# Kernel optimization log

Measured on AMD Instinct MI355X. Metric: run time of the kernel, lower is better.

The kernel has to match this reference:

```python
import jax, jax.numpy as jnp
import numpy as np

B, H, S, D = 4, 16, 2048, 128


def setup_inputs() -> dict:
    key = jax.random.key(0)
    kq, kk, kv, km = jax.random.split(key, 4)
    queries = jax.random.normal(kq, (B, H, S, D), dtype=jnp.float32)
    keys = jax.random.normal(kk, (B, H, S, D), dtype=jnp.float32)
    values = jax.random.normal(kv, (B, H, S, D), dtype=jnp.float32)
    # 0/1 float mask (1 = masked position), broadcast over heads
    mask = jax.random.randint(km, (B, 1, S, S), 0, 2).astype(jnp.float32)
    return {"queries": queries, "keys": keys, "values": values, "mask": mask}


def reference(queries, keys, values, mask):
    dk = jnp.asarray(keys.shape[-1], dtype=queries.dtype)
    # NOTE: original code divides by dk, not sqrt(dk) — kept faithful.
    scores = jnp.einsum("bhqd,bhkd->bhqk", queries, keys) / dk
    scores = scores + mask * jnp.asarray(-1e9, dtype=scores.dtype)
    attn = jax.nn.softmax(scores, axis=-1)
    out = jnp.einsum("bhqk,bhkd->bhqd", attn, values)
    return out, attn
```

## Files before the change

kernel.cpp:

```cpp
#include <hip/hip_runtime.h>

#define Bb 4
#define Hh 16
#define Ss 2048
#define Dd 128

typedef __bf16 bf16x8 __attribute__((ext_vector_type(8)));
typedef __bf16 bf16x4 __attribute__((ext_vector_type(4)));
typedef float f32x4 __attribute__((ext_vector_type(4)));

__global__ void k_cvt(const float4* __restrict__ Q, const float4* __restrict__ K,
                      bf16x4* __restrict__ Qb, bf16x4* __restrict__ Kb) {
    size_t i = (size_t)blockIdx.x * 256 + threadIdx.x;
    float4 q = Q[i], k = K[i];
    Qb[i] = (bf16x4){(__bf16)q.x, (__bf16)q.y, (__bf16)q.z, (__bf16)q.w};
    Kb[i] = (bf16x4){(__bf16)k.x, (__bf16)k.y, (__bf16)k.z, (__bf16)k.w};
}

__global__ void k_vt(const float* __restrict__ V, __bf16* __restrict__ VT) {
    __shared__ __bf16 lds[64][65];
    int k0 = blockIdx.x * 64, d0 = blockIdx.y * 64, bh = blockIdx.z;
    int t = threadIdx.x;
    for (int i = 0; i < 16; ++i) {
        int idx = i * 256 + t;
        int kl = idx >> 6, dl = idx & 63;
        lds[kl][dl] = (__bf16)V[((size_t)(bh * Ss + k0 + kl)) * Dd + d0 + dl];
    }
    __syncthreads();
    for (int i = 0; i < 16; ++i) {
        int idx = i * 256 + t;
        int dl = idx >> 6, kl = idx & 63;
        VT[((size_t)(bh * Dd + d0 + dl)) * Ss + k0 + kl] = lds[kl][dl];
    }
}

__global__ void k_mask(const float* __restrict__ M, unsigned* __restrict__ maskT) {
    __shared__ unsigned char lds[64][68];
    int k0 = blockIdx.x * 64, q0 = blockIdx.y * 64, b = blockIdx.z;
    int t = threadIdx.x;
    for (int i = 0; i < 16; ++i) {
        int idx = i * 256 + t;
        int ql = idx >> 6, kl = idx & 63;
        lds[ql][kl] = (M[((size_t)(b * Ss + q0 + ql)) * Ss + k0 + kl] != 0.0f) ? 1 : 0;
    }
    __syncthreads();
    if (t < 128) {
        int kl = t >> 1, wsel = t & 1;
        unsigned wv = 0;
        for (int j = 0; j < 32; ++j)
            wv |= ((unsigned)lds[wsel * 32 + j][kl]) << j;
        maskT[((size_t)(b * Ss + k0 + kl)) * (Ss / 32) + (q0 >> 5) + wsel] = wv;
    }
}

__global__ __launch_bounds__(256, 2) void attn_kernel(
    const __bf16* __restrict__ Qb, const __bf16* __restrict__ Kb,
    const __bf16* __restrict__ VTb, const unsigned* __restrict__ maskT,
    float* __restrict__ out, float* __restrict__ attn) {
    __shared__ __align__(16) __bf16 Qs[64][136];
    __shared__ __align__(16) __bf16 Ks[64][136];
    __shared__ __align__(16) __bf16 VTs[128][72];
    __shared__ __align__(16) __bf16 Ps[4][16][72];
    __shared__ float linv[64];

    const int t = threadIdx.x;
    const int w = t >> 6, lane = t & 63, quad = lane >> 4, l16 = lane & 15;
    const int bh = blockIdx.y, b = bh >> 4;
    const int q0 = blockIdx.x << 6;

    {
        const int row = t >> 4, col = (t & 15) << 3;
        for (int p = 0; p < 4; ++p) {
            int r = p * 16 + row;
            float4 v = *(const float4*)(Qb + ((size_t)(bh * Ss + q0 + r)) * Dd + col);
            *(float4*)&Qs[r][col] = v;
        }
    }
    const int qw = (q0 >> 5) + (w >> 1);
    const int bitbase = ((w & 1) << 4) + (quad << 2);

    __syncthreads();
    bf16x8 aq[4];
    for (int kd = 0; kd < 4; ++kd)
        aq[kd] = *(const bf16x8*)&Qs[w * 16 + l16][kd * 32 + quad * 8];

    float rsum[4] = {0.f, 0.f, 0.f, 0.f};

    for (int k0 = 0; k0 < Ss; k0 += 64) {
        __syncthreads();
        {
            const int row = t >> 4, col = (t & 15) << 3;
            for (int p = 0; p < 4; ++p) {
                int r = p * 16 + row;
                float4 v = *(const float4*)(Kb + ((size_t)(bh * Ss + k0 + r)) * Dd + col);
                *(float4*)&Ks[r][col] = v;
            }
        }
        __syncthreads();
        for (int nt = 0; nt < 4; ++nt) {
            f32x4 acc = {0.f, 0.f, 0.f, 0.f};
            for (int kd = 0; kd < 4; ++kd) {
                bf16x8 bk = *(const bf16x8*)&Ks[nt * 16 + l16][kd * 32 + quad * 8];
                acc = __builtin_amdgcn_mfma_f32_16x16x32_bf16(aq[kd], bk, acc, 0, 0, 0);
            }
            int col = k0 + nt * 16 + l16;
            unsigned mw = maskT[((size_t)(b * Ss + col)) * (Ss / 32) + qw];
            for (int r = 0; r < 4; ++r) {
                float p = ((mw >> (bitbase + r)) & 1u) ? 0.0f
                                                       : __expf(acc[r] * 0.0078125f);
                rsum[r] += p;
            }
        }
    }
    for (int r = 0; r < 4; ++r) {
        float v = rsum[r];
        v += __shfl_xor(v, 1, 16);
        v += __shfl_xor(v, 2, 16);
        v += __shfl_xor(v, 4, 16);
        v += __shfl_xor(v, 8, 16);
        rsum[r] = v;
    }
    if (l16 == 0)
        for (int r = 0; r < 4; ++r)
            linv[w * 16 + quad * 4 + r] = 1.0f / rsum[r];
    __syncthreads();
    float li[4];
    for (int r = 0; r < 4; ++r) li[r] = linv[w * 16 + quad * 4 + r];

    f32x4 oacc[8];
    for (int d = 0; d < 8; ++d) oacc[d] = (f32x4){0.f, 0.f, 0.f, 0.f};

    for (int k0 = 0; k0 < Ss; k0 += 64) {
        __syncthreads();
        {
            const int row = t >> 4, col = (t & 15) << 3;
            for (int p = 0; p < 4; ++p) {
                int r = p * 16 + row;
                float4 v = *(const float4*)(Kb + ((size_t)(bh * Ss + k0 + r)) * Dd + col);
                *(float4*)&Ks[r][col] = v;
            }
            const int vrow = t >> 3, vcol = (t & 7) << 3;
            for (int p = 0; p < 4; ++p) {
                int r = p * 32 + vrow;
                float4 v = *(const float4*)(VTb + ((size_t)(bh * Dd + r)) * Ss + k0 + vcol);
                *(float4*)&VTs[r][vcol] = v;
            }
        }
        __syncthreads();
        for (int nt = 0; nt < 4; ++nt) {
            f32x4 acc = {0.f, 0.f, 0.f, 0.f};
            for (int kd = 0; kd < 4; ++kd) {
                bf16x8 bk = *(const bf16x8*)&Ks[nt * 16 + l16][kd * 32 + quad * 8];
                acc = __builtin_amdgcn_mfma_f32_16x16x32_bf16(aq[kd], bk, acc, 0, 0, 0);
            }
            int col = k0 + nt * 16 + l16;
            unsigned mw = maskT[((size_t)(b * Ss + col)) * (Ss / 32) + qw];
            for (int r = 0; r < 4; ++r) {
                float p = ((mw >> (bitbase + r)) & 1u)
                              ? 0.0f
                              : __expf(acc[r] * 0.0078125f) * li[r];
                attn[((size_t)(bh * Ss + q0 + w * 16 + quad * 4 + r)) * Ss + col] = p;
                Ps[w][quad * 4 + r][nt * 16 + l16] = (__bf16)p;
            }
        }
        for (int kg = 0; kg < 2; ++kg) {
            bf16x8 ap = *(const bf16x8*)&Ps[w][l16][kg * 32 + quad * 8];
            for (int dg = 0; dg < 8; ++dg) {
                bf16x8 bv = *(const bf16x8*)&VTs[dg * 16 + l16][kg * 32 + quad * 8];
                oacc[dg] = __builtin_amdgcn_mfma_f32_16x16x32_bf16(ap, bv, oacc[dg], 0, 0, 0);
            }
        }
    }
    for (int dg = 0; dg < 8; ++dg)
        for (int r = 0; r < 4; ++r)
            out[((size_t)(bh * Ss + q0 + w * 16 + quad * 4 + r)) * Dd + dg * 16 + l16] =
                oacc[dg][r];
}

extern "C" void kernel_launch(void* const* d_in, const int* in_sizes, int n_in,
                              void* d_out, int out_size, void* d_ws, size_t ws_size,
                              hipStream_t stream) {
    const float* Q = (const float*)d_in[0];
    const float* K = (const float*)d_in[1];
    const float* V = (const float*)d_in[2];
    const float* M = (const float*)d_in[3];

    float* out = (float*)d_out;
    float* attn = out + (size_t)Bb * Hh * Ss * Dd;

    char* ws = (char*)d_ws;
    __bf16* Qb = (__bf16*)ws;
    __bf16* Kb = (__bf16*)(ws + 33554432);
    __bf16* VTb = (__bf16*)(ws + 67108864);
    unsigned* maskT = (unsigned*)(ws + 100663296);

    k_cvt<<<16384, 256, 0, stream>>>((const float4*)Q, (const float4*)K,
                                     (bf16x4*)Qb, (bf16x4*)Kb);
    k_vt<<<dim3(32, 2, 64), 256, 0, stream>>>(V, VTb);
    k_mask<<<dim3(32, 32, 4), 256, 0, stream>>>(M, maskT);
    attn_kernel<<<dim3(32, 64), 256, 0, stream>>>(Qb, Kb, VTb, maskT, out, attn);
}
```

Before: 1.813 ms.

## Double-buffer K/V tiles with direct global-to-LDS loads and swizzled layout

Rewrites the attention kernel's staging so K and V^T tiles of 32 keys are double-buffered in LDS and loaded with global_load_lds, letting the next tile's load run alongside the current tile's MFMAs. LDS rows are XOR-swizzled in place of padding, Q is loaded straight into registers, and the per-row reciprocal is computed in registers without an LDS round trip. Smaller LDS use allows 4 blocks per CU, and the workgroup index is remapped so neighbouring blocks share a head. The risks are more barriers per key, since the tiles are half as large, and higher register pressure under the tighter launch bound.

Measured after the change: 1.784 ms. No clear change (-1.6%).

```diff
diff --git a/kernel.cpp b/kernel.cpp
--- a/kernel.cpp
+++ b/kernel.cpp
@@ -4,6 +4,8 @@
 #define Hh 16
 #define Ss 2048
 #define Dd 128
+#define KT 32
+#define NIT (Ss / KT)
 
 typedef __bf16 bf16x8 __attribute__((ext_vector_type(8)));
 typedef __bf16 bf16x4 __attribute__((ext_vector_type(4)));
@@ -53,128 +55,169 @@
     }
 }
 
-__global__ __launch_bounds__(256, 2) void attn_kernel(
+__device__ __forceinline__ void gl2lds16(const void* g, void* l) {
+    __builtin_amdgcn_global_load_lds(
+        (const __attribute__((address_space(1))) unsigned int*)g,
+        (__attribute__((address_space(3))) unsigned int*)l, 16, 0, 0);
+}
+
+__global__ __launch_bounds__(256, 4) void attn_kernel(
     const __bf16* __restrict__ Qb, const __bf16* __restrict__ Kb,
     const __bf16* __restrict__ VTb, const unsigned* __restrict__ maskT,
     float* __restrict__ out, float* __restrict__ attn) {
-    __shared__ __align__(16) __bf16 Qs[64][136];
-    __shared__ __align__(16) __bf16 Ks[64][136];
-    __shared__ __align__(16) __bf16 VTs[128][72];
-    __shared__ __align__(16) __bf16 Ps[4][16][72];
-    __shared__ float linv[64];
+    __shared__ __align__(16) __bf16 Ks[2][KT][Dd];
+    __shared__ __align__(16) __bf16 VTs[2][Dd][KT];
+    __shared__ __align__(16) __bf16 Ps[4][16][64];
 
     const int t = threadIdx.x;
     const int w = t >> 6, lane = t & 63, quad = lane >> 4, l16 = lane & 15;
-    const int bh = blockIdx.y, b = bh >> 4;
-    const int q0 = blockIdx.x << 6;
-
+
+    const int wg = (int)blockIdx.x + ((int)blockIdx.y << 5);
+    const int nid = ((wg & 7) << 8) + (wg >> 3);
+    const int q0 = (nid & 31) << 6;
+    const int bh = nid >> 5;
+    const int b = bh >> 4;
+
+    const __bf16* Kbh = Kb + (size_t)bh * (Ss * Dd);
+    const char* Vbh = (const char*)(VTb + (size_t)bh * ((size_t)Dd * Ss));
+
+    const int ksub = t >> 4;
+    const int kcb = ((t & 15) << 4) ^ ((ksub & 7) << 4);
+    const int vsub = t >> 2;
+    const int vcb = ((t & 3) << 4) ^ ((vsub & 3) << 4);
+    char* ldsKbase = (char*)&Ks[0][0][0] + (w << 10);
+    char* ldsVbase = (char*)&VTs[0][0][0] + (w << 10);
+
+#define STAGE_K(buf, k0_)                                                      \
+    {                                                                          \
+        const char* gb = (const char*)(Kbh + (size_t)(k0_) * Dd) + kcb;        \
+        _Pragma("unroll") for (int i_ = 0; i_ < 2; ++i_)                       \
+            gl2lds16(gb + ((i_ << 4) + ksub) * 256,                            \
+                     ldsKbase + ((buf) << 13) + (i_ << 12));                   \
+    }
+#define STAGE_V(buf, k0_)                                                      \
+    {                                                                          \
+        const char* gb = Vbh + (size_t)(k0_) * 2 + vcb;                        \
+        _Pragma("unroll") for (int i_ = 0; i_ < 2; ++i_)                       \
+            gl2lds16(gb + (size_t)((i_ << 6) + vsub) * (Ss * 2),               \
+                     ldsVbase + ((buf) << 13) + (i_ << 12));                   \
+    }
+
+    bf16x8 aq[4];
     {
-        const int row = t >> 4, col = (t & 15) << 3;
-        for (int p = 0; p < 4; ++p) {
-            int r = p * 16 + row;
-            float4 v = *(const float4*)(Qb + ((size_t)(bh * Ss + q0 + r)) * Dd + col);
-            *(float4*)&Qs[r][col] = v;
-        }
-    }
+        STAGE_K(0, 0);
+        const __bf16* qp =
+            Qb + ((size_t)(bh * Ss + q0 + (w << 4) + l16)) * Dd + (quad << 3);
+#pragma unroll
+        for (int kd = 0; kd < 4; ++kd) aq[kd] = *(const bf16x8*)(qp + (kd << 5));
+    }
+    __syncthreads();
+
+    const char* ldsK0 = (const char*)&Ks[0][0][0];
+    const char* ldsV0 = (const char*)&VTs[0][0][0];
+    const int kswz = (l16 & 7) << 4;
+    const int vswz = (l16 & 3) << 4;
+
     const int qw = (q0 >> 5) + (w >> 1);
     const int bitbase = ((w & 1) << 4) + (quad << 2);
-
-    __syncthreads();
-    bf16x8 aq[4];
-    for (int kd = 0; kd < 4; ++kd)
-        aq[kd] = *(const bf16x8*)&Qs[w * 16 + l16][kd * 32 + quad * 8];
+    const size_t mrowbase = (size_t)b * Ss * (Ss / 32);
 
     float rsum[4] = {0.f, 0.f, 0.f, 0.f};
-
-    for (int k0 = 0; k0 < Ss; k0 += 64) {
+    for (int it = 0; it < NIT; ++it) {
+        const int cur = it & 1;
+        if (it < NIT - 1) {
+            STAGE_K(cur ^ 1, (it + 1) * KT);
+        } else {
+            STAGE_K(cur ^ 1, 0);
+            STAGE_V(cur ^ 1, 0);
+        }
+        const int k0 = it * KT;
+#pragma unroll
+        for (int nt = 0; nt < 2; ++nt) {
+            f32x4 acc = {0.f, 0.f, 0.f, 0.f};
+#pragma unroll
+            for (int kd = 0; kd < 4; ++kd) {
+                bf16x8 bk = *(const bf16x8*)(ldsK0 + (cur << 13) +
+                                             ((nt * 16 + l16) << 8) +
+                                             (((kd << 6) + (quad << 4)) ^ kswz));
+                acc = __builtin_amdgcn_mfma_f32_16x16x32_bf16(aq[kd], bk, acc, 0, 0, 0);
+            }
+            const int col = k0 + nt * 16 + l16;
+            const unsigned mw = maskT[mrowbase + (size_t)col * (Ss / 32) + qw];
+#pragma unroll
+            for (int r = 0; r < 4; ++r)
+                rsum[r] += ((mw >> (bitbase + r)) & 1u) ? 0.f
+                                                        : __expf(acc[r] * 0.0078125f);
+        }
         __syncthreads();
-        {
-            const int row = t >> 4, col = (t & 15) << 3;
-            for (int p = 0; p < 4; ++p) {
-                int r = p * 16 + row;
-                float4 v = *(const float4*)(Kb + ((size_t)(bh * Ss + k0 + r)) * Dd + col);
-                *(float4*)&Ks[r][col] = v;
-            }
-        }
-        __syncthreads();
-        for (int nt = 0; nt < 4; ++nt) {
-            f32x4 acc = {0.f, 0.f, 0.f, 0.f};
-            for (int kd = 0; kd < 4; ++kd) {
-                bf16x8 bk = *(const bf16x8*)&Ks[nt * 16 + l16][kd * 32 + quad * 8];
-                acc = __builtin_amdgcn_mfma_f32_16x16x32_bf16(aq[kd], bk, acc, 0, 0, 0);
-            }
-            int col = k0 + nt * 16 + l16;
-            unsigned mw = maskT[((size_t)(b * Ss + col)) * (Ss / 32) + qw];
-            for (int r = 0; r < 4; ++r) {
-                float p = ((mw >> (bitbase + r)) & 1u) ? 0.0f
-                                                       : __expf(acc[r] * 0.0078125f);
-                rsum[r] += p;
-            }
-        }
-    }
+    }
+
+    float li[4];
+#pragma unroll
     for (int r = 0; r < 4; ++r) {
         float v = rsum[r];
         v += __shfl_xor(v, 1, 16);
         v += __shfl_xor(v, 2, 16);
         v += __shfl_xor(v, 4, 16);
         v += __shfl_xor(v, 8, 16);
-        rsum[r] = v;
-    }
-    if (l16 == 0)
-        for (int r = 0; r < 4; ++r)
-            linv[w * 16 + quad * 4 + r] = 1.0f / rsum[r];
-    __syncthreads();
-    float li[4];
-    for (int r = 0; r < 4; ++r) li[r] = linv[w * 16 + quad * 4 + r];
+        li[r] = 1.0f / v;
+    }
 
     f32x4 oacc[8];
-    for (int d = 0; d < 8; ++d) oacc[d] = (f32x4){0.f, 0.f, 0.f, 0.f};
-
-    for (int k0 = 0; k0 < Ss; k0 += 64) {
-        __syncthreads();
-        {
-            const int row = t >> 4, col = (t & 15) << 3;
-            for (int p = 0; p < 4; ++p) {
-                int r = p * 16 + row;
-                float4 v = *(const float4*)(Kb + ((size_t)(bh * Ss + k0 + r)) * Dd + col);
-                *(float4*)&Ks[r][col] = v;
-            }
-            const int vrow = t >> 3, vcol = (t & 7) << 3;
-            for (int p = 0; p < 4; ++p) {
-                int r = p * 32 + vrow;
-                float4 v = *(const float4*)(VTb + ((size_t)(bh * Dd + r)) * Ss + k0 + vcol);
-                *(float4*)&VTs[r][vcol] = v;
-            }
-        }
-        __syncthreads();
-        for (int nt = 0; nt < 4; ++nt) {
+#pragma unroll
+    for (int dg = 0; dg < 8; ++dg) oacc[dg] = (f32x4){0.f, 0.f, 0.f, 0.f};
+
+    char* myPs = (char*)&Ps[0][0][0] + (w << 11);
+
+    for (int it = 0; it < NIT; ++it) {
+        const int cur = it & 1;
+        if (it < NIT - 1) {
+            STAGE_K(cur ^ 1, (it + 1) * KT);
+            STAGE_V(cur ^ 1, (it + 1) * KT);
+        }
+        const int k0 = it * KT;
+#pragma unroll
+        for (int nt = 0; nt < 2; ++nt) {
             f32x4 acc = {0.f, 0.f, 0.f, 0.f};
+#pragma unroll
             for (int kd = 0; kd < 4; ++kd) {
-                bf16x8 bk = *(const bf16x8*)&Ks[nt * 16 + l16][kd * 32 + quad * 8];
+                bf16x8 bk = *(const bf16x8*)(ldsK0 + (cur << 13) +
+                                             ((nt * 16 + l16) << 8) +
+                                             (((kd << 6) + (quad << 4)) ^ kswz));
                 acc = __builtin_amdgcn_mfma_f32_16x16x32_bf16(aq[kd], bk, acc, 0, 0, 0);
             }
-            int col = k0 + nt * 16 + l16;
-            unsigned mw = maskT[((size_t)(b * Ss + col)) * (Ss / 32) + qw];
+            const int col = k0 + nt * 16 + l16;
+            const unsigned mw = maskT[mrowbase + (size_t)col * (Ss / 32) + qw];
+#pragma unroll
             for (int r = 0; r < 4; ++r) {
+                const int prow = (quad << 2) + r;
                 float p = ((mw >> (bitbase + r)) & 1u)
                               ? 0.0f
                               : __expf(acc[r] * 0.0078125f) * li[r];
-                attn[((size_t)(bh * Ss + q0 + w * 16 + quad * 4 + r)) * Ss + col] = p;
-                Ps[w][quad * 4 + r][nt * 16 + l16] = (__bf16)p;
-            }
-        }
-        for (int kg = 0; kg < 2; ++kg) {
-            bf16x8 ap = *(const bf16x8*)&Ps[w][l16][kg * 32 + quad * 8];
+                attn[((size_t)(bh * Ss + q0 + (w << 4) + prow)) * Ss + col] = p;
+                *(__bf16*)(myPs + (prow << 7) +
+                           ((nt * 32 + (l16 << 1)) ^ ((prow & 7) << 4))) = (__bf16)p;
+            }
+        }
+        {
+            bf16x8 ap = *(const bf16x8*)(myPs + (l16 << 7) + ((quad << 4) ^ kswz));
+#pragma unroll
             for (int dg = 0; dg < 8; ++dg) {
-                bf16x8 bv = *(const bf16x8*)&VTs[dg * 16 + l16][kg * 32 + quad * 8];
+                bf16x8 bv = *(const bf16x8*)(ldsV0 + (cur << 13) +
+                                             ((dg * 16 + l16) << 6) +
+                                             ((quad << 4) ^ vswz));
                 oacc[dg] = __builtin_amdgcn_mfma_f32_16x16x32_bf16(ap, bv, oacc[dg], 0, 0, 0);
             }
         }
-    }
+        __syncthreads();
+    }
+
+#pragma unroll
     for (int dg = 0; dg < 8; ++dg)
+#pragma unroll
         for (int r = 0; r < 4; ++r)
-            out[((size_t)(bh * Ss + q0 + w * 16 + quad * 4 + r)) * Dd + dg * 16 + l16] =
-                oacc[dg][r];
+            out[((size_t)(bh * Ss + q0 + (w << 4) + (quad << 2) + r)) * Dd + dg * 16 +
+                l16] = oacc[dg][r];
 }
 
 extern "C" void kernel_launch(void* const* d_in, const int* in_sizes, int n_in,
```
